# Performance work log

Measured on AMD Instinct MI355X. Metric: run time of the kernel, lower is better.

The kernel has to match this reference:

```python
import jax, jax.numpy as jnp
import numpy as np

D_MODEL = 1024
N_HEADS = 16
D_K = D_MODEL // N_HEADS


def setup_inputs() -> dict:
    key = jax.random.key(0)
    k1, k2, k3 = jax.random.split(key, 3)
    x = jax.random.normal(k1, (2, 2048, D_MODEL), dtype=jnp.float32)
    # torch Linear(d, 3d).weight has shape [3d, d]; y = x @ W.T
    W_qkv = jax.random.normal(k2, (3 * D_MODEL, D_MODEL), dtype=jnp.float32) * (1.0 / np.sqrt(D_MODEL))
    W_out = jax.random.normal(k3, (D_MODEL, D_MODEL), dtype=jnp.float32) * (1.0 / np.sqrt(D_MODEL))
    return {"x": x, "W_qkv": W_qkv, "W_out": W_out}


def reference(x, W_qkv, W_out):
    batch, seq_len, d_model = x.shape
    qkv = jnp.einsum('bsd,ed->bse', x, W_qkv)  # [b, s, 3*d_model]
    qkv = qkv.reshape(batch, seq_len, 3, N_HEADS, D_K)
    qkv = jnp.transpose(qkv, (2, 0, 3, 1, 4))  # [3, b, h, s, dk]
    Q, K, V = qkv[0], qkv[1], qkv[2]
    scale = 1.0 / jnp.sqrt(jnp.asarray(D_K, dtype=x.dtype))
    scores = jnp.einsum('bhqd,bhkd->bhqk', Q, K) * scale  # [b, h, s, s]
    causal = jnp.tril(jnp.ones((seq_len, seq_len), dtype=bool))
    scores = jnp.where(causal, scores, jnp.asarray(-jnp.inf, dtype=scores.dtype))
    attn = jax.nn.softmax(scores, axis=-1)
    out = jnp.einsum('bhqk,bhkd->bhqd', attn, V)  # [b, h, s, dk]
    out = jnp.transpose(out, (0, 2, 1, 3)).reshape(batch, seq_len, d_model)
    return jnp.einsum('bsd,ed->bse', out, W_out)
```

## Files before the change

kernel.cpp:

```cpp
#include <hip/hip_runtime.h>
#include <stdint.h>

#define DMODEL 1024
#define NHEADS 16
#define DKH 64
#define BATCH 2
#define SEQ 2048
#define MTOT (BATCH*SEQ)

typedef __bf16 bf16x8 __attribute__((ext_vector_type(8)));
typedef __bf16 bf16x4 __attribute__((ext_vector_type(4)));
typedef float  f32x4  __attribute__((ext_vector_type(4)));

__device__ __forceinline__ f32x4 mfma16(bf16x8 a, bf16x8 b, f32x4 c){
  return __builtin_amdgcn_mfma_f32_16x16x32_bf16(a, b, c, 0, 0, 0);
}

__device__ __forceinline__ void gload_lds16(const void* g, void* l){
  __builtin_amdgcn_global_load_lds(
      (const __attribute__((address_space(1))) uint32_t*)(uintptr_t)g,
      (__attribute__((address_space(3))) uint32_t*)(uint32_t)(uintptr_t)l,
      16, 0, 0);
}

__device__ __forceinline__ unsigned short f2bf(float f){
  unsigned u = __builtin_bit_cast(unsigned, f);
  u += 0x7fff + ((u >> 16) & 1);
  return (unsigned short)(u >> 16);
}

#define QSCALE 0.1803368801111372f

__global__ void cvt3_kernel(const float* __restrict__ a, const float* __restrict__ b,
                            const float* __restrict__ c,
                            unsigned short* __restrict__ oa, unsigned short* __restrict__ ob,
                            unsigned short* __restrict__ oc,
                            int na4, int nb4, int nc4){
  int i = blockIdx.x * blockDim.x + threadIdx.x;
  const int tot = na4 + nb4 + nc4;
  const int stride = gridDim.x * blockDim.x;
  for (; i < tot; i += stride){
    const float4* s; ushort4* d; int k;
    if (i < na4)            { s = (const float4*)a; d = (ushort4*)oa; k = i; }
    else if (i < na4 + nb4) { s = (const float4*)b; d = (ushort4*)ob; k = i - na4; }
    else                    { s = (const float4*)c; d = (ushort4*)oc; k = i - na4 - nb4; }
    float4 v = s[k];
    ushort4 o;
    o.x = f2bf(v.x); o.y = f2bf(v.y); o.z = f2bf(v.z); o.w = f2bf(v.w);
    d[k] = o;
  }
}

template<int EPI, int BM, int BN, int NBN>
__global__ __launch_bounds__(256)
void gemm_bt(const __bf16* __restrict__ Ag, const __bf16* __restrict__ Bg,
             int M, int N, int K,
             __bf16* __restrict__ Qo, __bf16* __restrict__ Ko, __bf16* __restrict__ Vt,
             float* __restrict__ Co){
  constexpr int AM = BM/32;
  constexpr int AN = BN/32;
  constexpr int CA = BM/64;
  constexpr int CB = BN/64;
  __shared__ __align__(16) __bf16 As[2][BM*32];
  __shared__ __align__(16) __bf16 Bs[2][BN*32];
  const int tid  = threadIdx.x;
  const int wave = tid >> 6, lane = tid & 63;
  const int wr = wave >> 1, wc = wave & 1;
  const int lr = lane & 15, lg = lane >> 4;

  const int id  = blockIdx.x;
  const int xcd = id & 7;
  const int idx = id >> 3;
  const int m0  = (xcd*4 + idx/NBN) * BM;
  const int n0  = (idx % NBN) * BN;

  f32x4 acc[AM][AN] = {};

  const int srow = lane >> 2;
  const int scol = (lane & 3) * 8;
  const __bf16* gA = Ag + (size_t)(m0 + wave*(BM/4) + srow) * K + scol;
  const __bf16* gB = Bg + (size_t)(n0 + wave*(BN/4) + srow) * K + scol;

  const int nk = K >> 5;

#pragma unroll
  for (int c = 0; c < CA; c++)
    gload_lds16(gA + (size_t)(c*16)*K, &As[0][(wave*(BM/4) + c*16)*32]);
#pragma unroll
  for (int c = 0; c < CB; c++)
    gload_lds16(gB + (size_t)(c*16)*K, &Bs[0][(wave*(BN/4) + c*16)*32]);

  for (int t = 0; t < nk; t++){
    __syncthreads();
    if (t + 1 < nk){
      const int k0 = (t+1) << 5, bb = (t+1) & 1;
#pragma unroll
      for (int c = 0; c < CA; c++)
        gload_lds16(gA + k0 + (size_t)(c*16)*K, &As[bb][(wave*(BM/4) + c*16)*32]);
#pragma unroll
      for (int c = 0; c < CB; c++)
        gload_lds16(gB + k0 + (size_t)(c*16)*K, &Bs[bb][(wave*(BN/4) + c*16)*32]);
    }
    const int cb = t & 1;
    bf16x8 af[AM], bfv[AN];
#pragma unroll
    for (int i = 0; i < AM; i++)
      af[i] = *(const bf16x8*)&As[cb][(wr*(BM/2) + i*16 + lr)*32 + lg*8];
#pragma unroll
    for (int j = 0; j < AN; j++)
      bfv[j] = *(const bf16x8*)&Bs[cb][(wc*(BN/2) + j*16 + lr)*32 + lg*8];
#pragma unroll
    for (int i = 0; i < AM; i++)
#pragma unroll
      for (int j = 0; j < AN; j++)
        acc[i][j] = mfma16(af[i], bfv[j], acc[i][j]);
  }

  if (EPI == 0){
    const int three = n0 >> 10;
    if (three < 2){
#pragma unroll
      for (int i = 0; i < AM; i++){
#pragma unroll
        for (int j = 0; j < AN; j++){
#pragma unroll
          for (int r = 0; r < 4; r++){
            int m = m0 + wr*(BM/2) + i*16 + lg*4 + r;
            int n = n0 + wc*(BN/2) + j*16 + lr;
            int b = m >> 11, s = m & 2047;
            int h = (n >> 6) & 15, dk = n & 63;
            if (three == 0) Qo[(((size_t)(b*NHEADS + h))*SEQ + s)*DKH + dk] = (__bf16)(acc[i][j][r] * QSCALE);
            else            Ko[(((size_t)(b*NHEADS + h))*SEQ + s)*DKH + dk] = (__bf16)acc[i][j][r];
          }
        }
      }
    } else {
      __bf16 (*T)[136] = (__bf16(*)[136])&As[0][0];
      const int lrow = tid >> 3;
      const int mc   = (tid & 7) * 16;
      const int ngr  = (n0 - 2048) + ((lrow >> 4) << 6) + (lrow & 15);
      const int bb   = m0 >> 11;
      const int sbase= (m0 & 2047) + mc;
#pragma unroll
      for (int j = 0; j < AN; j++){
        __syncthreads();
#pragma unroll
        for (int i = 0; i < AM; i++){
          bf16x4 v;
#pragma unroll
          for (int r = 0; r < 4; r++) v[r] = (__bf16)acc[i][j][r];
          *(bf16x4*)&T[wc*16 + lr][wr*64 + i*16 + lg*4] = v;
        }
        __syncthreads();
        const int ng = ngr + j*16;
        __bf16* dst = Vt + (((size_t)(bb*NHEADS) + (ng >> 6))*DKH + (ng & 63))*SEQ + sbase;
        bf16x8 x0 = *(const bf16x8*)&T[lrow][mc];
        bf16x8 x1 = *(const bf16x8*)&T[lrow][mc + 8];
        *(bf16x8*)dst = x0;
        *(bf16x8*)(dst + 8) = x1;
      }
    }
  } else {
#pragma unroll
    for (int i = 0; i < AM; i++)
#pragma unroll
      for (int j = 0; j < AN; j++)
#pragma unroll
        for (int r = 0; r < 4; r++){
          int m = m0 + wr*(BM/2) + i*16 + lg*4 + r;
          int n = n0 + wc*(BN/2) + j*16 + lr;
          Co[(size_t)m * N + n] = acc[i][j][r];
        }
  }
}

__global__ __launch_bounds__(128)
void attn_kernel(const __bf16* __restrict__ Q, const __bf16* __restrict__ K,
                 const __bf16* __restrict__ Vt, __bf16* __restrict__ Aout){
  const int id   = blockIdx.x;
  const int xcd  = id & 7;
  const int slot = id >> 3;
  const int bh   = (xcd << 2) | (slot >> 5);
  const int j    = slot & 31;
  const int wave = threadIdx.x >> 6, lane = threadIdx.x & 63;
  const int lr = lane & 15, lg = lane >> 4;
  const int swz = (lr & 7) << 4;

  const __bf16* Qh = Q + (size_t)bh*SEQ*DKH;
  const char* Kc = (const char*)(K  + (size_t)bh*SEQ*DKH);
  const char* Vc = (const char*)(Vt + (size_t)bh*DKH*SEQ);

  __shared__ __align__(16) char lds[2][16384];

  const int row8 = lane >> 3;
  const int cG   = ((lane & 7) << 4) ^ (row8 << 4);

  const int b = bh >> 4, h = bh & 15;

  for (int ph = 0; ph < 2; ph++){
    const int tb  = ph ? (63 - j) : j;
    const int qw  = tb*32 + wave*16;
    const int nkv = (tb >> 1) + 1;

    bf16x8 qf0 = *(const bf16x8*)(Qh + (size_t)(qw + lr)*DKH + lg*8);
    bf16x8 qf1 = *(const bf16x8*)(Qh + (size_t)(qw + lr)*DKH + 32 + lg*8);

    f32x4 o[4] = {};
    float mrun = -1e30f, lrun = 0.f;

#pragma unroll
    for (int i = 0; i < 4; i++){
      const int srow = wave*32 + i*8 + row8;
      gload_lds16(Kc + (size_t)srow*128 + cG,  &lds[0][wave*4096 + i*1024]);
      gload_lds16(Vc + (size_t)srow*4096 + cG, &lds[0][8192 + wave*4096 + i*1024]);
    }
    __syncthreads();

    for (int kb = 0; kb < nkv; kb++){
      const int kv0 = kb*64;
      if (kb + 1 < nkv){
        const int nv0 = kv0 + 64;
#pragma unroll
        for (int i = 0; i < 4; i++){
          const int srow = wave*32 + i*8 + row8;
          gload_lds16(Kc + (size_t)(nv0 + srow)*128 + cG,
                      &lds[(kb+1)&1][wave*4096 + i*1024]);
          gload_lds16(Vc + (size_t)srow*4096 + (size_t)nv0*2 + cG,
                      &lds[(kb+1)&1][8192 + wave*4096 + i*1024]);
        }
      }
      const char* Ks = lds[kb&1];
      const char* Vs = lds[kb&1] + 8192;

      f32x4 sf[4];
      __builtin_amdgcn_s_setprio(1);
#pragma unroll
      for (int t = 0; t < 4; t++){
        const int row = t*16 + lr;
        bf16x8 kf0 = *(const bf16x8*)(Ks + row*128 + ((lg*16) ^ swz));
        bf16x8 kf1 = *(const bf16x8*)(Ks + row*128 + ((64 + lg*16) ^ swz));
        f32x4 c = {};
        c = mfma16(kf0, qf0, c);
        c = mfma16(kf1, qf1, c);
        sf[t] = c;
      }
      __builtin_amdgcn_s_setprio(0);
      if (kv0 + 63 > qw){
        const int q = qw + lr;
#pragma unroll
        for (int t = 0; t < 4; t++)
#pragma unroll
          for (int r = 0; r < 4; r++){
            int kv = kv0 + t*16 + lg*4 + r;
            sf[t][r] = (kv <= q) ? sf[t][r] : -1e30f;
          }
      }
      float mx = fmaxf(fmaxf(fmaxf(sf[0][0], sf[0][1]), fmaxf(sf[0][2], sf[0][3])),
                       fmaxf(fmaxf(sf[1][0], sf[1][1]), fmaxf(sf[1][2], sf[1][3])));
      float mx2 = fmaxf(fmaxf(fmaxf(sf[2][0], sf[2][1]), fmaxf(sf[2][2], sf[2][3])),
                        fmaxf(fmaxf(sf[3][0], sf[3][1]), fmaxf(sf[3][2], sf[3][3])));
      mx = fmaxf(mx, mx2);
      mx = fmaxf(mx, __shfl_xor(mx, 16));
      mx = fmaxf(mx, __shfl_xor(mx, 32));

      if (!__all(mx <= mrun + 8.0f)){
        float mn = fmaxf(mrun, mx);
        float alpha = __builtin_amdgcn_exp2f(mrun - mn);
        mrun = mn;
        lrun *= alpha;
        float av[4];
#pragma unroll
        for (int r = 0; r < 4; r++) av[r] = __shfl(alpha, lg*4 + r);
#pragma unroll
        for (int n = 0; n < 4; n++)
#pragma unroll
          for (int r = 0; r < 4; r++) o[n][r] *= av[r];
      }

      float p[16];
#pragma unroll
      for (int t = 0; t < 4; t++)
#pragma unroll
        for (int r = 0; r < 4; r++){
          float v = __builtin_amdgcn_exp2f(sf[t][r] - mrun);
          p[t*4 + r] = v;
          lrun += v;
        }

      bf16x8 pa0, pa1;
#pragma unroll
      for (int i = 0; i < 8; i++){ pa0[i] = (__bf16)p[i]; pa1[i] = (__bf16)p[8 + i]; }
      __builtin_amdgcn_s_setprio(1);
#pragma unroll
      for (int n = 0; n < 4; n++){
        const int row = n*16 + lr;
        bf16x4 vlo0 = *(const bf16x4*)(Vs + row*128 + ((lg*8) ^ swz));
        bf16x4 vhi0 = *(const bf16x4*)(Vs + row*128 + ((32 + lg*8) ^ swz));
        bf16x4 vlo1 = *(const bf16x4*)(Vs + row*128 + ((64 + lg*8) ^ swz));
        bf16x4 vhi1 = *(const bf16x4*)(Vs + row*128 + ((96 + lg*8) ^ swz));
        bf16x8 vf0 = __builtin_shufflevector(vlo0, vhi0, 0,1,2,3,4,5,6,7);
        bf16x8 vf1 = __builtin_shufflevector(vlo1, vhi1, 0,1,2,3,4,5,6,7);
        o[n] = mfma16(pa0, vf0, o[n]);
        o[n] = mfma16(pa1, vf1, o[n]);
      }
      __builtin_amdgcn_s_setprio(0);
      __syncthreads();
    }

    lrun += __shfl_xor(lrun, 16);
    lrun += __shfl_xor(lrun, 32);
    float inv = 1.0f / lrun;
#pragma unroll
    for (int r = 0; r < 4; r++){
      float invr = __shfl(inv, lg*4 + r);
      __bf16* dst = Aout + ((size_t)b*SEQ + qw + lg*4 + r)*DMODEL + h*DKH;
#pragma unroll
      for (int n = 0; n < 4; n++)
        dst[n*16 + lr] = (__bf16)(o[n][r] * invr);
    }
  }
}

extern "C" void kernel_launch(void* const* d_in, const int* in_sizes, int n_in,
                              void* d_out, int out_size, void* d_ws, size_t ws_size,
                              hipStream_t stream){
  const float* x    = (const float*)d_in[0];
  const float* wqkv = (const float*)d_in[1];
  const float* wout = (const float*)d_in[2];
  float* out = (float*)d_out;
  char* ws = (char*)d_ws;

  __bf16* xb  = (__bf16*)(ws);
  __bf16* Ab  = (__bf16*)(ws);
  __bf16* wqb = (__bf16*)(ws + 8388608);
  __bf16* wob = (__bf16*)(ws + 14680064);
  __bf16* Qb  = (__bf16*)(ws + 16777216);
  __bf16* Kb  = (__bf16*)(ws + 25165824);
  __bf16* Vtb = (__bf16*)(ws + 33554432);

  cvt3_kernel<<<2048, 256, 0, stream>>>(x, wqkv, wout,
                                        (unsigned short*)xb, (unsigned short*)wqb, (unsigned short*)wob,
                                        (MTOT*DMODEL)/4, (3*DMODEL*DMODEL)/4, (DMODEL*DMODEL)/4);

  gemm_bt<0,128,128,24><<<768, 256, 0, stream>>>(xb, wqb, MTOT, 3*DMODEL, DMODEL,
                                                 Qb, Kb, Vtb, nullptr);
  attn_kernel<<<1024, 128, 0, stream>>>(Qb, Kb, Vtb, Ab);
  gemm_bt<1,128,64,16><<<512, 256, 0, stream>>>(Ab, wob, MTOT, DMODEL, DMODEL,
                                                nullptr, nullptr, nullptr, out);
}
```

Baseline: 173.0 us.

## Restructure attention: one tile per block, register-staged single LDS buffer, MFMA row sums

```diff
diff --git a/kernel.cpp b/kernel.cpp
--- a/kernel.cpp
+++ b/kernel.cpp
@@ -174,14 +174,14 @@
   }
 }
 
-__global__ __launch_bounds__(128)
+__global__ __launch_bounds__(128, 4)
 void attn_kernel(const __bf16* __restrict__ Q, const __bf16* __restrict__ K,
                  const __bf16* __restrict__ Vt, __bf16* __restrict__ Aout){
   const int id   = blockIdx.x;
   const int xcd  = id & 7;
   const int slot = id >> 3;
-  const int bh   = (xcd << 2) | (slot >> 5);
-  const int j    = slot & 31;
+  const int bh   = (xcd << 2) | (slot >> 6);
+  const int tb   = 63 - (slot & 63);
   const int wave = threadIdx.x >> 6, lane = threadIdx.x & 63;
   const int lr = lane & 15, lg = lane >> 4;
   const int swz = (lr & 7) << 4;
@@ -190,134 +190,143 @@
   const char* Kc = (const char*)(K  + (size_t)bh*SEQ*DKH);
   const char* Vc = (const char*)(Vt + (size_t)bh*DKH*SEQ);
 
-  __shared__ __align__(16) char lds[2][16384];
+  __shared__ __align__(16) char lds[16384];
 
   const int row8 = lane >> 3;
-  const int cG   = ((lane & 7) << 4) ^ (row8 << 4);
+  const int cL   = (lane & 7) << 4;
+  const int cW   = cL ^ (row8 << 4);
 
   const int b = bh >> 4, h = bh & 15;
-
-  for (int ph = 0; ph < 2; ph++){
-    const int tb  = ph ? (63 - j) : j;
-    const int qw  = tb*32 + wave*16;
-    const int nkv = (tb >> 1) + 1;
-
-    bf16x8 qf0 = *(const bf16x8*)(Qh + (size_t)(qw + lr)*DKH + lg*8);
-    bf16x8 qf1 = *(const bf16x8*)(Qh + (size_t)(qw + lr)*DKH + 32 + lg*8);
-
-    f32x4 o[4] = {};
-    float mrun = -1e30f, lrun = 0.f;
-
-#pragma unroll
-    for (int i = 0; i < 4; i++){
-      const int srow = wave*32 + i*8 + row8;
-      gload_lds16(Kc + (size_t)srow*128 + cG,  &lds[0][wave*4096 + i*1024]);
-      gload_lds16(Vc + (size_t)srow*4096 + cG, &lds[0][8192 + wave*4096 + i*1024]);
-    }
+  const int qw  = tb*32 + wave*16;
+  const int nkv = (tb >> 1) + 1;
+
+  bf16x8 qf0 = *(const bf16x8*)(Qh + (size_t)(qw + lr)*DKH + lg*8);
+  bf16x8 qf1 = *(const bf16x8*)(Qh + (size_t)(qw + lr)*DKH + 32 + lg*8);
+
+  bf16x8 ONE8;
+#pragma unroll
+  for (int i = 0; i < 8; i++) ONE8[i] = (__bf16)1.0f;
+
+  f32x4 o[4] = {};
+  f32x4 lac = {};
+  float mrun = -1e30f;
+
+  int4 kr[4], vr[4];
+#pragma unroll
+  for (int c = 0; c < 4; c++){
+    const int row = wave*32 + c*8 + row8;
+    kr[c] = *(const int4*)(Kc + (size_t)row*128 + cL);
+    vr[c] = *(const int4*)(Vc + (size_t)row*4096 + cL);
+  }
+
+  for (int kb = 0; kb < nkv; kb++){
+    const int kv0 = kb*64;
     __syncthreads();
-
-    for (int kb = 0; kb < nkv; kb++){
-      const int kv0 = kb*64;
-      if (kb + 1 < nkv){
-        const int nv0 = kv0 + 64;
-#pragma unroll
-        for (int i = 0; i < 4; i++){
-          const int srow = wave*32 + i*8 + row8;
-          gload_lds16(Kc + (size_t)(nv0 + srow)*128 + cG,
-                      &lds[(kb+1)&1][wave*4096 + i*1024]);
-          gload_lds16(Vc + (size_t)srow*4096 + (size_t)nv0*2 + cG,
-                      &lds[(kb+1)&1][8192 + wave*4096 + i*1024]);
+#pragma unroll
+    for (int c = 0; c < 4; c++){
+      const int row = wave*32 + c*8 + row8;
+      *(int4*)(&lds[row*128 + cW]) = kr[c];
+      *(int4*)(&lds[8192 + row*128 + cW]) = vr[c];
+    }
+    if (kb + 1 < nkv){
+      const int nv0 = kv0 + 64;
+#pragma unroll
+      for (int c = 0; c < 4; c++){
+        const int row = wave*32 + c*8 + row8;
+        kr[c] = *(const int4*)(Kc + (size_t)(nv0 + row)*128 + cL);
+        vr[c] = *(const int4*)(Vc + (size_t)row*4096 + (size_t)nv0*2 + cL);
+      }
+    }
+    __syncthreads();
+    const char* Ks = lds;
+    const char* Vs = lds + 8192;
+
+    f32x4 sf[4];
+    __builtin_amdgcn_s_setprio(1);
+#pragma unroll
+    for (int t = 0; t < 4; t++){
+      const int row = t*16 + lr;
+      bf16x8 kf0 = *(const bf16x8*)(Ks + row*128 + ((lg*16) ^ swz));
+      bf16x8 kf1 = *(const bf16x8*)(Ks + row*128 + ((64 + lg*16) ^ swz));
+      f32x4 c = {};
+      c = mfma16(kf0, qf0, c);
+      c = mfma16(kf1, qf1, c);
+      sf[t] = c;
+    }
+    __builtin_amdgcn_s_setprio(0);
+    if (kv0 + 63 > qw){
+      const int q = qw + lr;
+#pragma unroll
+      for (int t = 0; t < 4; t++)
+#pragma unroll
+        for (int r = 0; r < 4; r++){
+          int kv = kv0 + t*16 + lg*4 + r;
+          sf[t][r] = (kv <= q) ? sf[t][r] : -1e30f;
         }
-      }
-      const char* Ks = lds[kb&1];
-      const char* Vs = lds[kb&1] + 8192;
-
-      f32x4 sf[4];
-      __builtin_amdgcn_s_setprio(1);
-#pragma unroll
-      for (int t = 0; t < 4; t++){
-        const int row = t*16 + lr;
-        bf16x8 kf0 = *(const bf16x8*)(Ks + row*128 + ((lg*16) ^ swz));
-        bf16x8 kf1 = *(const bf16x8*)(Ks + row*128 + ((64 + lg*16) ^ swz));
-        f32x4 c = {};
-        c = mfma16(kf0, qf0, c);
-        c = mfma16(kf1, qf1, c);
-        sf[t] = c;
-      }
-      __builtin_amdgcn_s_setprio(0);
-      if (kv0 + 63 > qw){
-        const int q = qw + lr;
-#pragma unroll
-        for (int t = 0; t < 4; t++)
-#pragma unroll
-          for (int r = 0; r < 4; r++){
-            int kv = kv0 + t*16 + lg*4 + r;
-            sf[t][r] = (kv <= q) ? sf[t][r] : -1e30f;
-          }
-      }
-      float mx = fmaxf(fmaxf(fmaxf(sf[0][0], sf[0][1]), fmaxf(sf[0][2], sf[0][3])),
-                       fmaxf(fmaxf(sf[1][0], sf[1][1]), fmaxf(sf[1][2], sf[1][3])));
-      float mx2 = fmaxf(fmaxf(fmaxf(sf[2][0], sf[2][1]), fmaxf(sf[2][2], sf[2][3])),
-                        fmaxf(fmaxf(sf[3][0], sf[3][1]), fmaxf(sf[3][2], sf[3][3])));
-      mx = fmaxf(mx, mx2);
-      mx = fmaxf(mx, __shfl_xor(mx, 16));
-      mx = fmaxf(mx, __shfl_xor(mx, 32));
-
-      if (!__all(mx <= mrun + 8.0f)){
-        float mn = fmaxf(mrun, mx);
-        float alpha = __builtin_amdgcn_exp2f(mrun - mn);
-        mrun = mn;
-        lrun *= alpha;
-        float av[4];
-#pragma unroll
-        for (int r = 0; r < 4; r++) av[r] = __shfl(alpha, lg*4 + r);
-#pragma unroll
-        for (int n = 0; n < 4; n++)
-#pragma unroll
-          for (int r = 0; r < 4; r++) o[n][r] *= av[r];
-      }
-
-      float p[16];
-#pragma unroll
-      for (int t = 0; t < 4; t++)
-#pragma unroll
-        for (int r = 0; r < 4; r++){
-          float v = __builtin_amdgcn_exp2f(sf[t][r] - mrun);
-          p[t*4 + r] = v;
-          lrun += v;
-        }
-
-      bf16x8 pa0, pa1;
-#pragma unroll
-      for (int i = 0; i < 8; i++){ pa0[i] = (__bf16)p[i]; pa1[i] = (__bf16)p[8 + i]; }
-      __builtin_amdgcn_s_setprio(1);
-#pragma unroll
-      for (int n = 0; n < 4; n++){
-        const int row = n*16 + lr;
-        bf16x4 vlo0 = *(const bf16x4*)(Vs + row*128 + ((lg*8) ^ swz));
-        bf16x4 vhi0 = *(const bf16x4*)(Vs + row*128 + ((32 + lg*8) ^ swz));
-        bf16x4 vlo1 = *(const bf16x4*)(Vs + row*128 + ((64 + lg*8) ^ swz));
-        bf16x4 vhi1 = *(const bf16x4*)(Vs + row*128 + ((96 + lg*8) ^ swz));
-        bf16x8 vf0 = __builtin_shufflevector(vlo0, vhi0, 0,1,2,3,4,5,6,7);
-        bf16x8 vf1 = __builtin_shufflevector(vlo1, vhi1, 0,1,2,3,4,5,6,7);
-        o[n] = mfma16(pa0, vf0, o[n]);
-        o[n] = mfma16(pa1, vf1, o[n]);
-      }
-      __builtin_amdgcn_s_setprio(0);
-      __syncthreads();
-    }
-
-    lrun += __shfl_xor(lrun, 16);
-    lrun += __shfl_xor(lrun, 32);
-    float inv = 1.0f / lrun;
-#pragma unroll
-    for (int r = 0; r < 4; r++){
-      float invr = __shfl(inv, lg*4 + r);
-      __bf16* dst = Aout + ((size_t)b*SEQ + qw + lg*4 + r)*DMODEL + h*DKH;
+    }
+    float ma = fmaxf(fmaxf(sf[0][0], sf[0][1]), sf[0][2]);
+    float mb = fmaxf(fmaxf(sf[0][3], sf[1][0]), sf[1][1]);
+    float mc = fmaxf(fmaxf(sf[1][2], sf[1][3]), sf[2][0]);
+    float md = fmaxf(fmaxf(sf[2][1], sf[2][2]), sf[2][3]);
+    float me = fmaxf(fmaxf(sf[3][0], sf[3][1]), sf[3][2]);
+    float mx = fmaxf(fmaxf(ma, mb), mc);
+    mx = fmaxf(fmaxf(mx, md), me);
+    mx = fmaxf(mx, sf[3][3]);
+    mx = fmaxf(mx, __shfl_xor(mx, 16));
+    mx = fmaxf(mx, __shfl_xor(mx, 32));
+
+    if (!__all(mx <= mrun + 8.0f)){
+      float mn = fmaxf(mrun, mx);
+      float alpha = __builtin_amdgcn_exp2f(mrun - mn);
+      mrun = mn;
+      float av[4];
+#pragma unroll
+      for (int r = 0; r < 4; r++) av[r] = __shfl(alpha, lg*4 + r);
 #pragma unroll
       for (int n = 0; n < 4; n++)
-        dst[n*16 + lr] = (__bf16)(o[n][r] * invr);
-    }
+#pragma unroll
+        for (int r = 0; r < 4; r++) o[n][r] *= av[r];
+#pragma unroll
+      for (int r = 0; r < 4; r++) lac[r] *= av[r];
+    }
+
+    bf16x8 pa0, pa1;
+#pragma unroll
+    for (int t = 0; t < 2; t++)
+#pragma unroll
+      for (int r = 0; r < 4; r++)
+        pa0[t*4 + r] = (__bf16)__builtin_amdgcn_exp2f(sf[t][r] - mrun);
+#pragma unroll
+    for (int t = 0; t < 2; t++)
+#pragma unroll
+      for (int r = 0; r < 4; r++)
+        pa1[t*4 + r] = (__bf16)__builtin_amdgcn_exp2f(sf[t+2][r] - mrun);
+
+    __builtin_amdgcn_s_setprio(1);
+    lac = mfma16(pa0, ONE8, lac);
+    lac = mfma16(pa1, ONE8, lac);
+#pragma unroll
+    for (int n = 0; n < 4; n++){
+      const int row = n*16 + lr;
+      bf16x4 vlo0 = *(const bf16x4*)(Vs + row*128 + ((lg*8) ^ swz));
+      bf16x4 vhi0 = *(const bf16x4*)(Vs + row*128 + ((32 + lg*8) ^ swz));
+      bf16x4 vlo1 = *(const bf16x4*)(Vs + row*128 + ((64 + lg*8) ^ swz));
+      bf16x4 vhi1 = *(const bf16x4*)(Vs + row*128 + ((96 + lg*8) ^ swz));
+      bf16x8 vf0 = __builtin_shufflevector(vlo0, vhi0, 0,1,2,3,4,5,6,7);
+      bf16x8 vf1 = __builtin_shufflevector(vlo1, vhi1, 0,1,2,3,4,5,6,7);
+      o[n] = mfma16(pa0, vf0, o[n]);
+      o[n] = mfma16(pa1, vf1, o[n]);
+    }
+    __builtin_amdgcn_s_setprio(0);
+  }
+
+#pragma unroll
+  for (int r = 0; r < 4; r++){
+    float invr = 1.0f / lac[r];
+    __bf16* dst = Aout + ((size_t)b*SEQ + qw + lg*4 + r)*DMODEL + h*DKH;
+#pragma unroll
+    for (int n = 0; n < 4; n++)
+      dst[n*16 + lr] = (__bf16)(o[n][r] * invr);
   }
 }
 
@@ -344,7 +353,7 @@
 
   gemm_bt<0,128,128,24><<<768, 256, 0, stream>>>(xb, wqb, MTOT, 3*DMODEL, DMODEL,
                                                  Qb, Kb, Vtb, nullptr);
-  attn_kernel<<<1024, 128, 0, stream>>>(Qb, Kb, Vtb, Ab);
+  attn_kernel<<<2048, 128, 0, stream>>>(Qb, Kb, Vtb, Ab);
   gemm_bt<1,128,64,16><<<512, 256, 0, stream>>>(Ab, wob, MTOT, DMODEL, DMODEL,
                                                 nullptr, nullptr, nullptr, out);
 }
```

Measured after the change: 338.5 us. 95.7% more time.
